# Performance work log

Hardware: AMD Instinct MI355X
Metric: run time of the kernel (lower is better)

The kernel has to match this reference:

```python
import jax, jax.numpy as jnp
import numpy as np

N_NODES = 50000
NUM_FEATURE = 256
NUM_HIDDEN = 128
NUM_CLASSES = 16
N_EDGES = 1600000


def gcn_conv(x, W, b, src, dst, deg_inv_sqrt, n_nodes):
    # GCNConv: h = x @ W ; out[i] = sum_{j->i} norm_ji * h[j] + b
    # with symmetric normalization over the self-loop-augmented graph.
    h = x @ W  # [N, out_ch]
    norm = deg_inv_sqrt[src] * deg_inv_sqrt[dst]  # [E']
    msgs = h[src] * norm[:, None]  # [E', out_ch] (dominant intermediate)
    out = jax.ops.segment_sum(msgs, dst, num_segments=n_nodes)
    return out + b


def setup_inputs() -> dict:
    key = jax.random.key(0)
    k_x, k_e, k_w1, k_b1, k_w2, k_b2 = jax.random.split(key, 6)
    x = jax.random.normal(k_x, (N_NODES, NUM_FEATURE), dtype=jnp.float32)
    edge_index = jax.random.randint(k_e, (2, N_EDGES), 0, N_NODES, dtype=jnp.int64)
    # Glorot init like PyG's GCNConv linear
    s1 = (6.0 / (NUM_FEATURE + NUM_HIDDEN)) ** 0.5
    s2 = (6.0 / (NUM_HIDDEN + NUM_CLASSES)) ** 0.5
    W1 = jax.random.uniform(k_w1, (NUM_FEATURE, NUM_HIDDEN), jnp.float32, -s1, s1)
    b1 = jnp.zeros((NUM_HIDDEN,), jnp.float32)
    W2 = jax.random.uniform(k_w2, (NUM_HIDDEN, NUM_CLASSES), jnp.float32, -s2, s2)
    b2 = jnp.zeros((NUM_CLASSES,), jnp.float32)
    return {"x": x, "edge_index": edge_index, "W1": W1, "b1": b1, "W2": W2, "b2": b2}


def reference(x, edge_index, W1, b1, W2, b2):
    n = x.shape[0]
    # add self-loops (done inside GCNConv for each layer; identical both times)
    loops = jnp.arange(n, dtype=edge_index.dtype)
    src = jnp.concatenate([edge_index[0], loops])
    dst = jnp.concatenate([edge_index[1], loops])
    deg = jax.ops.segment_sum(jnp.ones_like(dst, dtype=x.dtype), dst, num_segments=n)
    deg_inv_sqrt = jnp.where(deg > 0, jax.lax.rsqrt(deg), 0.0)

    h = jax.nn.relu(gcn_conv(x, W1, b1, src, dst, deg_inv_sqrt, n))
    # F.dropout with training=False is the identity (eval-mode baseline)
    logits = gcn_conv(h, W2, b2, src, dst, deg_inv_sqrt, n)
    return jax.nn.log_softmax(logits, axis=1)
```

## Files before the change

kernel.cpp:

```cpp
#include <hip/hip_runtime.h>
#include <hip/hip_fp16.h>
#include <math.h>

#define NF 256
#define NH 128
#define NC 16
#define NB 391
#define NBLK 512

typedef __attribute__((ext_vector_type(8))) short bf16x8;
typedef __attribute__((ext_vector_type(4))) float f32x4;

__device__ __forceinline__ unsigned f2b(float f) {
    unsigned u = __float_as_uint(f);
    return (u + 0x7FFFu + ((u >> 16) & 1u)) >> 16;
}
__device__ __forceinline__ unsigned packt(float a, float b) {
    return (__float_as_uint(a) >> 16) | (__float_as_uint(b) & 0xFFFF0000u);
}
union h2u { __half2 h; unsigned u; };
__device__ __forceinline__ __half2 uh(unsigned u) { h2u c; c.u = u; return c.h; }

__global__ void passA_kernel(const int* __restrict__ dst, int* __restrict__ hist, int E) {
    __shared__ int h[NB];
    for (int i = threadIdx.x; i < NB; i += 256) h[i] = 0;
    __syncthreads();
    int b = blockIdx.x;
    int e0 = (int)((long long)b * E / NBLK), e1 = (int)((long long)(b + 1) * E / NBLK);
    for (int e = e0 + (int)threadIdx.x; e < e1; e += 256)
        atomicAdd(&h[dst[e] >> 7], 1);
    __syncthreads();
    for (int i = threadIdx.x; i < NB; i += 256) hist[b * NB + i] = h[i];
}

__global__ void scanR_kernel(const int* __restrict__ hist, int* __restrict__ bsum) {
    __shared__ int sm[NBLK];
    int k = blockIdx.x, t = threadIdx.x;
    sm[t] = hist[t * NB + k];
    __syncthreads();
    for (int off = NBLK / 2; off > 0; off >>= 1) {
        if (t < off) sm[t] += sm[t + off];
        __syncthreads();
    }
    if (t == 0) bsum[k] = sm[0];
}

__global__ void scanB_kernel(const int* __restrict__ bsum, int* __restrict__ ubase,
                             int* __restrict__ pbase, int N, int E) {
    __shared__ int smu[512];
    __shared__ int smp[512];
    int t = threadIdx.x;
    int vu = (t < NB) ? bsum[t] : 0;
    int vp = (t < NB) ? (((vu + 7) & ~7) + 904) : 0;
    smu[t] = vu; smp[t] = vp;
    __syncthreads();
    for (int off = 1; off < 512; off <<= 1) {
        int uu = (t >= off) ? smu[t - off] : 0;
        int pp = (t >= off) ? smp[t - off] : 0;
        __syncthreads();
        smu[t] += uu; smp[t] += pp;
        __syncthreads();
    }
    if (t < NB) { ubase[t] = smu[t] - vu; pbase[t] = smp[t] - vp; }
    if (t == 0) ubase[NB] = E;
}

__global__ void scanC_kernel(int* __restrict__ hist, const int* __restrict__ ubase) {
    __shared__ int sm[NBLK];
    int k = blockIdx.x, t = threadIdx.x;
    int v = hist[t * NB + k];
    sm[t] = v;
    __syncthreads();
    for (int off = 1; off < NBLK; off <<= 1) {
        int u = (t >= off) ? sm[t - off] : 0;
        __syncthreads();
        sm[t] += u;
        __syncthreads();
    }
    hist[t * NB + k] = ubase[k] + sm[t] - v;
}

__global__ void passB_kernel(const int* __restrict__ src, const int* __restrict__ dst,
                             const int* __restrict__ hist, unsigned* __restrict__ ebuf,
                             int E) {
    __shared__ int cur[NB];
    int b = blockIdx.x;
    for (int i = threadIdx.x; i < NB; i += 256) cur[i] = hist[b * NB + i];
    __syncthreads();
    int e0 = (int)((long long)b * E / NBLK), e1 = (int)((long long)(b + 1) * E / NBLK);
    for (int e = e0 + (int)threadIdx.x; e < e1; e += 256) {
        int d = dst[e];
        int pos = atomicAdd(&cur[d >> 7], 1);
        ebuf[pos] = ((unsigned)d << 16) | (unsigned)src[e];
    }
}

__global__ void passC_kernel(const unsigned* __restrict__ ebuf, const int* __restrict__ ubase,
                             const int* __restrict__ pbase, int* __restrict__ rowptr,
                             int* __restrict__ degs, float* __restrict__ dis,
                             unsigned short* __restrict__ colidx, int N) {
    __shared__ int h[128];
    __shared__ int s2[128];
    __shared__ int curp[128];
    int k = blockIdx.x, t = threadIdx.x;
    if (t < 128) h[t] = 0;
    __syncthreads();
    int e0 = ubase[k], e1 = ubase[k + 1];
    for (int e = e0 + t; e < e1; e += 256)
        atomicAdd(&h[(ebuf[e] >> 16) & 127], 1);
    __syncthreads();
    int v = (t < 128) ? h[t] : 0;
    int pd = (v + 7) & ~7;
    if (t < 128) s2[t] = pd;
    __syncthreads();
    for (int off = 1; off < 128; off <<= 1) {
        int u = (t < 128 && t >= off) ? s2[t - off] : 0;
        __syncthreads();
        if (t < 128) s2[t] += u;
        __syncthreads();
    }
    if (t < 128) {
        int start = pbase[k] + s2[t] - pd;
        int node = k * 128 + t;
        if (node < N) {
            rowptr[node] = start;
            degs[node] = v;
            dis[node] = rsqrtf((float)(v + 1));
        }
        curp[t] = start;
    }
    __syncthreads();
    for (int e = e0 + t; e < e1; e += 256) {
        unsigned w = ebuf[e];
        int dl = (w >> 16) & 127;
        int pos = atomicAdd(&curp[dl], 1);
        colidx[pos] = (unsigned short)(w & 0xFFFFu);
    }
    __syncthreads();
    if (t < 128) {
        int endp = pbase[k] + s2[t];
        for (int q = curp[t]; q < endp; ++q) colidx[q] = (unsigned short)N;
    }
}

__global__ void w1t_kernel(const float* __restrict__ W1, unsigned short* __restrict__ W1T,
                           unsigned* __restrict__ h1T, unsigned* __restrict__ h2sb, int N) {
    int idx = blockIdx.x * 256 + threadIdx.x;
    int n = idx >> 8, k = idx & 255;
    W1T[n * 256 + k] = (unsigned short)f2b(W1[(size_t)k * NH + n]);
    if (idx < 64) {
        int p = idx >> 4, j = idx & 15;
        h1T[(size_t)p * (N + 1) * 16 + (size_t)N * 16 + j] = 0u;
    } else if (idx < 72) {
        h2sb[(size_t)N * 8 + (idx - 64)] = 0u;
    }
}

__global__ __launch_bounds__(256) void gemm1_mfma_kernel(
    const float* __restrict__ x, const unsigned short* __restrict__ W1T,
    const float* __restrict__ dis, unsigned short* __restrict__ h1us, int N) {
    __shared__ char sx[32768];
    int tid = threadIdx.x;
    int wid = tid >> 6, lane = tid & 63;

    for (int it = 0; it < 8; ++it) {
        int lr = it * 4 + wid;
        int grow = blockIdx.x * 32 + lr;
        if (grow >= N) grow = N - 1;
        int fsw = (lr & 7) << 1;
        const char* gp = (const char*)x + (size_t)grow * 1024 + ((lane ^ fsw) << 4);
        __builtin_amdgcn_global_load_lds(gp, sx + lr * 1024 + lane * 16, 16, 0, 0);
    }
    __syncthreads();

    int lrow = lane & 15, lk = lane >> 4;
    int rt = wid & 1, nh = wid >> 1;
    int lr = rt * 16 + lrow;
    int fr = (lr & 7) << 1;
    const float4* lds4 = (const float4*)sx;

    bf16x8 a[8];
#pragma unroll
    for (int kk = 0; kk < 8; ++kk) {
        int v = (kk * 8 + lk * 2) ^ fr;
        float4 lo = lds4[lr * 64 + v];
        float4 hi = lds4[lr * 64 + v + 1];
        union { unsigned u[4]; bf16x8 vv; } av;
        av.u[0] = packt(lo.x, lo.y);
        av.u[1] = packt(lo.z, lo.w);
        av.u[2] = packt(hi.x, hi.y);
        av.u[3] = packt(hi.z, hi.w);
        a[kk] = av.vv;
    }

    f32x4 acc[4];
#pragma unroll
    for (int t = 0; t < 4; ++t) acc[t] = (f32x4){0.f, 0.f, 0.f, 0.f};

#pragma unroll
    for (int nt = 0; nt < 4; ++nt) {
        int n = nh * 64 + nt * 16 + lrow;
        const unsigned short* wp = W1T + (size_t)n * 256 + lk * 8;
        bf16x8 b0 = *(const bf16x8*)(wp + 0 * 32);
        bf16x8 b1 = *(const bf16x8*)(wp + 1 * 32);
        bf16x8 b2 = *(const bf16x8*)(wp + 2 * 32);
        bf16x8 b3 = *(const bf16x8*)(wp + 3 * 32);
        bf16x8 b4 = *(const bf16x8*)(wp + 4 * 32);
        bf16x8 b5 = *(const bf16x8*)(wp + 5 * 32);
        bf16x8 b6 = *(const bf16x8*)(wp + 6 * 32);
        bf16x8 b7 = *(const bf16x8*)(wp + 7 * 32);
        acc[nt] = __builtin_amdgcn_mfma_f32_16x16x32_bf16(a[0], b0, acc[nt], 0, 0, 0);
        acc[nt] = __builtin_amdgcn_mfma_f32_16x16x32_bf16(a[1], b1, acc[nt], 0, 0, 0);
        acc[nt] = __builtin_amdgcn_mfma_f32_16x16x32_bf16(a[2], b2, acc[nt], 0, 0, 0);
        acc[nt] = __builtin_amdgcn_mfma_f32_16x16x32_bf16(a[3], b3, acc[nt], 0, 0, 0);
        acc[nt] = __builtin_amdgcn_mfma_f32_16x16x32_bf16(a[4], b4, acc[nt], 0, 0, 0);
        acc[nt] = __builtin_amdgcn_mfma_f32_16x16x32_bf16(a[5], b5, acc[nt], 0, 0, 0);
        acc[nt] = __builtin_amdgcn_mfma_f32_16x16x32_bf16(a[6], b6, acc[nt], 0, 0, 0);
        acc[nt] = __builtin_amdgcn_mfma_f32_16x16x32_bf16(a[7], b7, acc[nt], 0, 0, 0);
    }

    int rb = blockIdx.x * 32;
    int crow0 = rb + rt * 16 + lk * 4;
#pragma unroll
    for (int r = 0; r < 4; ++r) {
        int row = crow0 + r;
        if (row < N) {
            float dr = dis[row];
#pragma unroll
            for (int nt = 0; nt < 4; ++nt) {
                int p = nh * 2 + (nt >> 1);
                size_t ad = ((size_t)p * (N + 1) + row) * 32 + ((nt & 1) * 16 + lrow);
                __half hv = __float2half(acc[nt][r] * dr);
                h1us[ad] = __half_as_ushort(hv);
            }
        }
    }
}

__global__ __launch_bounds__(256) void aggall_kernel(
    const int* __restrict__ rowptr, const int* __restrict__ degs,
    const unsigned short* __restrict__ colidx,
    const __half2* __restrict__ h1T, __half2* __restrict__ aggT, int N, int bps) {
    int p = blockIdx.x / bps;
    int i = (blockIdx.x - p * bps) * 16 + (threadIdx.x >> 4);
    if (i >= N) return;
    int l = threadIdx.x & 15;
    const __half2* slab = h1T + (size_t)p * (N + 1) * 16;
    __half2 acc = slab[(size_t)i * 16 + l];
    int e = rowptr[i];
    int cnt8 = (degs[i] + 7) >> 3;
    int npair = cnt8 >> 1;
    if (npair > 0) {
        uint4 w0 = *reinterpret_cast<const uint4*>(colidx + e);
        uint4 w1 = *reinterpret_cast<const uint4*>(colidx + e + 8);
        for (int b = 1; b < npair; ++b) {
            uint4 n0 = *reinterpret_cast<const uint4*>(colidx + e + 16 * b);
            uint4 n1 = *reinterpret_cast<const uint4*>(colidx + e + 16 * b + 8);
            int a0 = w0.x & 0xFFFF, a1 = w0.x >> 16, a2 = w0.y & 0xFFFF, a3 = w0.y >> 16;
            int a4 = w0.z & 0xFFFF, a5 = w0.z >> 16, a6 = w0.w & 0xFFFF, a7 = w0.w >> 16;
            int c0 = w1.x & 0xFFFF, c1 = w1.x >> 16, c2 = w1.y & 0xFFFF, c3 = w1.y >> 16;
            int c4 = w1.z & 0xFFFF, c5 = w1.z >> 16, c6 = w1.w & 0xFFFF, c7 = w1.w >> 16;
            __half2 v0 = slab[(size_t)a0 * 16 + l];
            __half2 v1 = slab[(size_t)a1 * 16 + l];
            __half2 v2 = slab[(size_t)a2 * 16 + l];
            __half2 v3 = slab[(size_t)a3 * 16 + l];
            __half2 v4 = slab[(size_t)a4 * 16 + l];
            __half2 v5 = slab[(size_t)a5 * 16 + l];
            __half2 v6 = slab[(size_t)a6 * 16 + l];
            __half2 v7 = slab[(size_t)a7 * 16 + l];
            __half2 u0 = slab[(size_t)c0 * 16 + l];
            __half2 u1 = slab[(size_t)c1 * 16 + l];
            __half2 u2 = slab[(size_t)c2 * 16 + l];
            __half2 u3 = slab[(size_t)c3 * 16 + l];
            __half2 u4 = slab[(size_t)c4 * 16 + l];
            __half2 u5 = slab[(size_t)c5 * 16 + l];
            __half2 u6 = slab[(size_t)c6 * 16 + l];
            __half2 u7 = slab[(size_t)c7 * 16 + l];
            __half2 s0 = __hadd2(__hadd2(v0, v1), __hadd2(v2, v3));
            __half2 s1 = __hadd2(__hadd2(v4, v5), __hadd2(v6, v7));
            __half2 s2 = __hadd2(__hadd2(u0, u1), __hadd2(u2, u3));
            __half2 s3 = __hadd2(__hadd2(u4, u5), __hadd2(u6, u7));
            acc = __hadd2(acc, __hadd2(__hadd2(s0, s1), __hadd2(s2, s3)));
            w0 = n0; w1 = n1;
        }
        {
            int a0 = w0.x & 0xFFFF, a1 = w0.x >> 16, a2 = w0.y & 0xFFFF, a3 = w0.y >> 16;
            int a4 = w0.z & 0xFFFF, a5 = w0.z >> 16, a6 = w0.w & 0xFFFF, a7 = w0.w >> 16;
            int c0 = w1.x & 0xFFFF, c1 = w1.x >> 16, c2 = w1.y & 0xFFFF, c3 = w1.y >> 16;
            int c4 = w1.z & 0xFFFF, c5 = w1.z >> 16, c6 = w1.w & 0xFFFF, c7 = w1.w >> 16;
            __half2 v0 = slab[(size_t)a0 * 16 + l];
            __half2 v1 = slab[(size_t)a1 * 16 + l];
            __half2 v2 = slab[(size_t)a2 * 16 + l];
            __half2 v3 = slab[(size_t)a3 * 16 + l];
            __half2 v4 = slab[(size_t)a4 * 16 + l];
            __half2 v5 = slab[(size_t)a5 * 16 + l];
            __half2 v6 = slab[(size_t)a6 * 16 + l];
            __half2 v7 = slab[(size_t)a7 * 16 + l];
            __half2 u0 = slab[(size_t)c0 * 16 + l];
            __half2 u1 = slab[(size_t)c1 * 16 + l];
            __half2 u2 = slab[(size_t)c2 * 16 + l];
            __half2 u3 = slab[(size_t)c3 * 16 + l];
            __half2 u4 = slab[(size_t)c4 * 16 + l];
            __half2 u5 = slab[(size_t)c5 * 16 + l];
            __half2 u6 = slab[(size_t)c6 * 16 + l];
            __half2 u7 = slab[(size_t)c7 * 16 + l];
            __half2 s0 = __hadd2(__hadd2(v0, v1), __hadd2(v2, v3));
            __half2 s1 = __hadd2(__hadd2(v4, v5), __hadd2(v6, v7));
            __half2 s2 = __hadd2(__hadd2(u0, u1), __hadd2(u2, u3));
            __half2 s3 = __hadd2(__hadd2(u4, u5), __hadd2(u6, u7));
            acc = __hadd2(acc, __hadd2(__hadd2(s0, s1), __hadd2(s2, s3)));
        }
        e += npair * 16;
    }
    if (cnt8 & 1) {
        uint4 w = *reinterpret_cast<const uint4*>(colidx + e);
        int a0 = w.x & 0xFFFF, a1 = w.x >> 16, a2 = w.y & 0xFFFF, a3 = w.y >> 16;
        int a4 = w.z & 0xFFFF, a5 = w.z >> 16, a6 = w.w & 0xFFFF, a7 = w.w >> 16;
        __half2 v0 = slab[(size_t)a0 * 16 + l];
        __half2 v1 = slab[(size_t)a1 * 16 + l];
        __half2 v2 = slab[(size_t)a2 * 16 + l];
        __half2 v3 = slab[(size_t)a3 * 16 + l];
        __half2 v4 = slab[(size_t)a4 * 16 + l];
        __half2 v5 = slab[(size_t)a5 * 16 + l];
        __half2 v6 = slab[(size_t)a6 * 16 + l];
        __half2 v7 = slab[(size_t)a7 * 16 + l];
        __half2 s01 = __hadd2(v0, v1), s23 = __hadd2(v2, v3);
        __half2 s45 = __hadd2(v4, v5), s67 = __hadd2(v6, v7);
        acc = __hadd2(acc, __hadd2(__hadd2(s01, s23), __hadd2(s45, s67)));
    }
    aggT[(size_t)p * N * 16 + (size_t)i * 16 + l] = acc;
}

__global__ __launch_bounds__(256) void relu_gemm2_kernel(
    const __half2* __restrict__ aggT, const float* __restrict__ dis,
    const float* __restrict__ b1, const float* __restrict__ W2,
    __half2* __restrict__ h2sb, int N) {
    __shared__ float sW2[NH * NC];
    __shared__ float srow[4][NH];
    int tid = threadIdx.x;
    for (int k = tid; k < NH * NC; k += 256) sW2[k] = W2[k];
    __syncthreads();

    int wid = tid >> 6, lane = tid & 63;
    int i = blockIdx.x * 4 + wid;
    if (i >= N) return;
    int p = lane >> 4, l16 = lane & 15;
    float2 f = __half22float2(aggT[((size_t)p * N + i) * 16 + l16]);
    float di = dis[i];
    int c0 = p * 32 + l16 * 2;
    srow[wid][c0]     = fmaxf(di * f.x + b1[c0], 0.f);
    srow[wid][c0 + 1] = fmaxf(di * f.y + b1[c0 + 1], 0.f);
    int j = lane & 15, q = lane >> 4;
    const float* rw = srow[wid];
    float pacc = 0.f;
#pragma unroll
    for (int cc = 0; cc < 32; ++cc) {
        int c = q * 32 + cc;
        pacc += rw[c] * sW2[c * NC + j];
    }
    pacc += __shfl_xor(pacc, 16, 64);
    pacc += __shfl_xor(pacc, 32, 64);
    float dp = di * pacc;
    float plo = __shfl(dp, (lane << 1) & 63, 64);
    float phi = __shfl(dp, ((lane << 1) | 1) & 63, 64);
    if (lane < 8) h2sb[(size_t)i * 8 + lane] = __floats2half2_rn(plo, phi);
}

__global__ void layer2_kernel(const int* __restrict__ rowptr, const int* __restrict__ degs,
                              const unsigned short* __restrict__ colidx,
                              const uint2* __restrict__ h2sb2, const float* __restrict__ dis,
                              const float* __restrict__ b2, float* __restrict__ out, int N) {
    int t = blockIdx.x * 256 + threadIdx.x;
    int i = t >> 2;
    if (i >= N) return;
    int j4 = t & 3;
    int e = rowptr[i];
    int cnt4 = (degs[i] + 3) >> 2;
    uint2 sv = h2sb2[(size_t)i * 4 + j4];
    __half2 acc0 = uh(sv.x), acc1 = uh(sv.y);
    if (cnt4 > 0) {
        uint2 w = *reinterpret_cast<const uint2*>(colidx + e);
        for (int b = 1; b < cnt4; ++b) {
            uint2 wn = *reinterpret_cast<const uint2*>(colidx + e + 4 * b);
            int a0 = w.x & 0xFFFF, a1 = w.x >> 16;
            int a2 = w.y & 0xFFFF, a3 = w.y >> 16;
            uint2 g0 = h2sb2[(size_t)a0 * 4 + j4];
            uint2 g1 = h2sb2[(size_t)a1 * 4 + j4];
            uint2 g2 = h2sb2[(size_t)a2 * 4 + j4];
            uint2 g3 = h2sb2[(size_t)a3 * 4 + j4];
            acc0 = __hadd2(acc0, __hadd2(__hadd2(uh(g0.x), uh(g1.x)),
                                         __hadd2(uh(g2.x), uh(g3.x))));
            acc1 = __hadd2(acc1, __hadd2(__hadd2(uh(g0.y), uh(g1.y)),
                                         __hadd2(uh(g2.y), uh(g3.y))));
            w = wn;
        }
        int a0 = w.x & 0xFFFF, a1 = w.x >> 16;
        int a2 = w.y & 0xFFFF, a3 = w.y >> 16;
        uint2 g0 = h2sb2[(size_t)a0 * 4 + j4];
        uint2 g1 = h2sb2[(size_t)a1 * 4 + j4];
        uint2 g2 = h2sb2[(size_t)a2 * 4 + j4];
        uint2 g3 = h2sb2[(size_t)a3 * 4 + j4];
        acc0 = __hadd2(acc0, __hadd2(__hadd2(uh(g0.x), uh(g1.x)),
                                     __hadd2(uh(g2.x), uh(g3.x))));
        acc1 = __hadd2(acc1, __hadd2(__hadd2(uh(g0.y), uh(g1.y)),
                                     __hadd2(uh(g2.y), uh(g3.y))));
    }
    float2 f0 = __half22float2(acc0);
    float2 f1 = __half22float2(acc1);
    float di = dis[i];
    float4 bb = *reinterpret_cast<const float4*>(b2 + 4 * j4);
    float l0 = di * f0.x + bb.x;
    float l1 = di * f0.y + bb.y;
    float l2 = di * f1.x + bb.z;
    float l3 = di * f1.y + bb.w;
    float m = fmaxf(fmaxf(l0, l1), fmaxf(l2, l3));
    m = fmaxf(m, __shfl_xor(m, 1, 64));
    m = fmaxf(m, __shfl_xor(m, 2, 64));
    float s = __expf(l0 - m) + __expf(l1 - m) + __expf(l2 - m) + __expf(l3 - m);
    s += __shfl_xor(s, 1, 64);
    s += __shfl_xor(s, 2, 64);
    float lse = m + __logf(s);
    float4 o = make_float4(l0 - lse, l1 - lse, l2 - lse, l3 - lse);
    *reinterpret_cast<float4*>(out + (size_t)i * NC + 4 * j4) = o;
}

extern "C" void kernel_launch(void* const* d_in, const int* in_sizes, int n_in,
                              void* d_out, int out_size, void* d_ws, size_t ws_size,
                              hipStream_t stream) {
    const float* x  = (const float*)d_in[0];
    const int*   ei = (const int*)d_in[1];
    const float* W1 = (const float*)d_in[2];
    const float* b1 = (const float*)d_in[3];
    const float* W2 = (const float*)d_in[4];
    const float* b2 = (const float*)d_in[5];
    float* out = (float*)d_out;

    const int N = in_sizes[0] / NF;
    const int E = in_sizes[1] / 2;
    const int* src = ei;
    const int* dst = ei + E;

    __half2*        h1T    = (__half2*)d_ws;
    __half2*        aggT   = h1T + (size_t)4 * (N + 1) * 16;
    __half2*        h2sb   = aggT + (size_t)4 * N * 16;
    float*          dis    = (float*)(h2sb + (size_t)(N + 1) * 8);
    int*            degs   = (int*)(dis + N);
    int*            rowptr = degs + N;
    int*            hist   = rowptr + N;
    int*            bsum   = hist + NBLK * NB;
    int*            ubase  = bsum + NB;
    int*            pbase  = ubase + NB + 1;
    unsigned*       ebuf   = (unsigned*)(pbase + NB + 1);
    unsigned short* colidx = (unsigned short*)(ebuf + E);
    unsigned short* W1T    = (unsigned short*)ebuf;

    passA_kernel<<<NBLK, 256, 0, stream>>>(dst, hist, E);
    scanR_kernel<<<NB, NBLK, 0, stream>>>(hist, bsum);
    scanB_kernel<<<1, 512, 0, stream>>>(bsum, ubase, pbase, N, E);
    scanC_kernel<<<NB, NBLK, 0, stream>>>(hist, ubase);
    passB_kernel<<<NBLK, 256, 0, stream>>>(src, dst, hist, ebuf, E);
    passC_kernel<<<NB, 256, 0, stream>>>(ebuf, ubase, pbase, rowptr, degs, dis, colidx, N);

    w1t_kernel<<<128, 256, 0, stream>>>(W1, W1T, (unsigned*)h1T, (unsigned*)h2sb, N);

    gemm1_mfma_kernel<<<(N + 31) / 32, 256, 0, stream>>>(x, W1T, dis,
                                                         (unsigned short*)h1T, N);

    const int bps = (N + 15) / 16;
    aggall_kernel<<<4 * bps, 256, 0, stream>>>(rowptr, degs, colidx, h1T, aggT, N, bps);

    relu_gemm2_kernel<<<(N + 3) / 4, 256, 0, stream>>>(aggT, dis, b1, W2, h2sb, N);

    layer2_kernel<<<((size_t)N * 4 + 255) / 256, 256, 0, stream>>>(rowptr, degs, colidx,
                                                                   (const uint2*)h2sb, dis, b2, out, N);
}
```

Before: 164.4 us.

## Pre-convert x to fp16 in fused prep kernel and use f16 MFMA GEMM1

Merges the edge histogram pass and the W1 transpose into one prep launch, which also converts x to fp16 into workspace when space allows. GEMM1 then reads half-width x and uses f16 MFMA instead of converting fp32 x itself. The x conversion overlaps with the histogram blocks and is meant to halve GEMM1's input traffic and cut one launch. The cost is an extra full read and write of x, an fp16 range/precision risk, and a fallback that depends on the workspace size.

Result: no change. 166.5 us (+1.3%).

```diff
diff --git a/kernel.cpp b/kernel.cpp
--- a/kernel.cpp
+++ b/kernel.cpp
@@ -7,8 +7,10 @@
 #define NC 16
 #define NB 391
 #define NBLK 512
+#define XCB 512
 
 typedef __attribute__((ext_vector_type(8))) short bf16x8;
+typedef __attribute__((ext_vector_type(8))) _Float16 f16x8;
 typedef __attribute__((ext_vector_type(4))) float f32x4;
 
 __device__ __forceinline__ unsigned f2b(float f) {
@@ -20,17 +22,44 @@
 }
 union h2u { __half2 h; unsigned u; };
 __device__ __forceinline__ __half2 uh(unsigned u) { h2u c; c.u = u; return c.h; }
-
-__global__ void passA_kernel(const int* __restrict__ dst, int* __restrict__ hist, int E) {
+__device__ __forceinline__ unsigned hu(__half2 h) { h2u c; c.h = h; return c.u; }
+
+__global__ void prep_kernel(const int* __restrict__ dst, int* __restrict__ hist, int E,
+                            const float* __restrict__ W1, unsigned short* __restrict__ W1T,
+                            unsigned* __restrict__ h1T, unsigned* __restrict__ h2sb,
+                            const float* __restrict__ x, uint2* __restrict__ xh,
+                            int N, int C4, int fast) {
     __shared__ int h[NB];
-    for (int i = threadIdx.x; i < NB; i += 256) h[i] = 0;
-    __syncthreads();
-    int b = blockIdx.x;
-    int e0 = (int)((long long)b * E / NBLK), e1 = (int)((long long)(b + 1) * E / NBLK);
-    for (int e = e0 + (int)threadIdx.x; e < e1; e += 256)
-        atomicAdd(&h[dst[e] >> 7], 1);
-    __syncthreads();
-    for (int i = threadIdx.x; i < NB; i += 256) hist[b * NB + i] = h[i];
+    int b = blockIdx.x, tid = threadIdx.x;
+    if (b < NBLK) {
+        for (int i = tid; i < NB; i += 256) h[i] = 0;
+        __syncthreads();
+        int e0 = (int)((long long)b * E / NBLK), e1 = (int)((long long)(b + 1) * E / NBLK);
+        for (int e = e0 + tid; e < e1; e += 256)
+            atomicAdd(&h[dst[e] >> 7], 1);
+        __syncthreads();
+        for (int i = tid; i < NB; i += 256) hist[b * NB + i] = h[i];
+    } else if (b < NBLK + 128) {
+        int idx = (b - NBLK) * 256 + tid;
+        int n = idx >> 8, k = idx & 255;
+        float w = W1[(size_t)k * NH + n];
+        W1T[n * 256 + k] = fast ? __half_as_ushort(__float2half(w))
+                                : (unsigned short)f2b(w);
+        if (idx < 64) {
+            int p = idx >> 4, j = idx & 15;
+            h1T[(size_t)p * (N + 1) * 16 + (size_t)N * 16 + j] = 0u;
+        } else if (idx < 72) {
+            h2sb[(size_t)N * 8 + (idx - 64)] = 0u;
+        }
+    } else if (fast) {
+        int i = (b - NBLK - 128) * 256 + tid;
+        const float4* x4 = (const float4*)x;
+        for (; i < C4; i += XCB * 256) {
+            float4 v = x4[i];
+            xh[i] = make_uint2(hu(__floats2half2_rn(v.x, v.y)),
+                               hu(__floats2half2_rn(v.z, v.w)));
+        }
+    }
 }
 
 __global__ void scanR_kernel(const int* __restrict__ hist, int* __restrict__ bsum) {
@@ -143,20 +172,81 @@
     }
 }
 
-__global__ void w1t_kernel(const float* __restrict__ W1, unsigned short* __restrict__ W1T,
-                           unsigned* __restrict__ h1T, unsigned* __restrict__ h2sb, int N) {
-    int idx = blockIdx.x * 256 + threadIdx.x;
-    int n = idx >> 8, k = idx & 255;
-    W1T[n * 256 + k] = (unsigned short)f2b(W1[(size_t)k * NH + n]);
-    if (idx < 64) {
-        int p = idx >> 4, j = idx & 15;
-        h1T[(size_t)p * (N + 1) * 16 + (size_t)N * 16 + j] = 0u;
-    } else if (idx < 72) {
-        h2sb[(size_t)N * 8 + (idx - 64)] = 0u;
-    }
-}
-
-__global__ __launch_bounds__(256) void gemm1_mfma_kernel(
+__global__ __launch_bounds__(256) void gemm1_f16_kernel(
+    const unsigned short* __restrict__ xh, const unsigned short* __restrict__ W1T,
+    const float* __restrict__ dis, unsigned short* __restrict__ h1us, int N) {
+    __shared__ char sx[16384];
+    int tid = threadIdx.x;
+    int wid = tid >> 6, lane = tid & 63;
+
+    for (int it = 0; it < 4; ++it) {
+        int rp = (it * 4 + wid) * 2;
+        int row = rp + (lane >> 5);
+        int grow = blockIdx.x * 32 + row;
+        if (grow >= N) grow = N - 1;
+        int u = (lane & 31) ^ (row & 7);
+        const char* gp = (const char*)(xh + (size_t)grow * 256) + (u << 4);
+        __builtin_amdgcn_global_load_lds(gp, sx + rp * 512 + lane * 16, 16, 0, 0);
+    }
+    __syncthreads();
+
+    int lrow = lane & 15, lk = lane >> 4;
+    int rt = wid & 1, nh = wid >> 1;
+    int lr = rt * 16 + lrow;
+    int sw = lr & 7;
+
+    f16x8 a[8];
+#pragma unroll
+    for (int kk = 0; kk < 8; ++kk) {
+        int u = (kk * 4 + lk) ^ sw;
+        a[kk] = *(const f16x8*)(sx + lr * 512 + u * 16);
+    }
+
+    f32x4 acc[4];
+#pragma unroll
+    for (int t = 0; t < 4; ++t) acc[t] = (f32x4){0.f, 0.f, 0.f, 0.f};
+
+#pragma unroll
+    for (int nt = 0; nt < 4; ++nt) {
+        int n = nh * 64 + nt * 16 + lrow;
+        const unsigned short* wp = W1T + (size_t)n * 256 + lk * 8;
+        f16x8 b0 = *(const f16x8*)(wp + 0 * 32);
+        f16x8 b1 = *(const f16x8*)(wp + 1 * 32);
+        f16x8 b2 = *(const f16x8*)(wp + 2 * 32);
+        f16x8 b3 = *(const f16x8*)(wp + 3 * 32);
+        f16x8 b4 = *(const f16x8*)(wp + 4 * 32);
+        f16x8 b5 = *(const f16x8*)(wp + 5 * 32);
+        f16x8 b6 = *(const f16x8*)(wp + 6 * 32);
+        f16x8 b7 = *(const f16x8*)(wp + 7 * 32);
+        acc[nt] = __builtin_amdgcn_mfma_f32_16x16x32_f16(a[0], b0, acc[nt], 0, 0, 0);
+        acc[nt] = __builtin_amdgcn_mfma_f32_16x16x32_f16(a[1], b1, acc[nt], 0, 0, 0);
+        acc[nt] = __builtin_amdgcn_mfma_f32_16x16x32_f16(a[2], b2, acc[nt], 0, 0, 0);
+        acc[nt] = __builtin_amdgcn_mfma_f32_16x16x32_f16(a[3], b3, acc[nt], 0, 0, 0);
+        acc[nt] = __builtin_amdgcn_mfma_f32_16x16x32_f16(a[4], b4, acc[nt], 0, 0, 0);
+        acc[nt] = __builtin_amdgcn_mfma_f32_16x16x32_f16(a[5], b5, acc[nt], 0, 0, 0);
+        acc[nt] = __builtin_amdgcn_mfma_f32_16x16x32_f16(a[6], b6, acc[nt], 0, 0, 0);
+        acc[nt] = __builtin_amdgcn_mfma_f32_16x16x32_f16(a[7], b7, acc[nt], 0, 0, 0);
+    }
+
+    int rb = blockIdx.x * 32;
+    int crow0 = rb + rt * 16 + lk * 4;
+#pragma unroll
+    for (int r = 0; r < 4; ++r) {
+        int row = crow0 + r;
+        if (row < N) {
+            float dr = dis[row];
+#pragma unroll
+            for (int nt = 0; nt < 4; ++nt) {
+                int p = nh * 2 + (nt >> 1);
+                size_t ad = ((size_t)p * (N + 1) + row) * 32 + ((nt & 1) * 16 + lrow);
+                __half hv = __float2half(acc[nt][r] * dr);
+                h1us[ad] = __half_as_ushort(hv);
+            }
+        }
+    }
+}
+
+__global__ __launch_bounds__(256) void gemm1_f32_kernel(
     const float* __restrict__ x, const unsigned short* __restrict__ W1T,
     const float* __restrict__ dis, unsigned short* __restrict__ h1us, int N) {
     __shared__ char sx[32768];
@@ -452,19 +542,28 @@
     int*            pbase  = ubase + NB + 1;
     unsigned*       ebuf   = (unsigned*)(pbase + NB + 1);
     unsigned short* colidx = (unsigned short*)(ebuf + E);
-    unsigned short* W1T    = (unsigned short*)ebuf;
-
-    passA_kernel<<<NBLK, 256, 0, stream>>>(dst, hist, E);
+    unsigned short* W1T    = colidx + (size_t)E + 360000;
+    size_t off_xh = (((size_t)((char*)(W1T + 32768) - (char*)d_ws)) + 15) & ~(size_t)15;
+    unsigned short* xh     = (unsigned short*)((char*)d_ws + off_xh);
+    size_t need_fast = off_xh + (size_t)N * 256 * sizeof(unsigned short);
+    int fast = (ws_size >= need_fast) ? 1 : 0;
+    const int C4 = N * NF / 4;
+
+    prep_kernel<<<NBLK + 128 + XCB, 256, 0, stream>>>(dst, hist, E, W1, W1T,
+                                                      (unsigned*)h1T, (unsigned*)h2sb,
+                                                      x, (uint2*)xh, N, C4, fast);
     scanR_kernel<<<NB, NBLK, 0, stream>>>(hist, bsum);
     scanB_kernel<<<1, 512, 0, stream>>>(bsum, ubase, pbase, N, E);
     scanC_kernel<<<NB, NBLK, 0, stream>>>(hist, ubase);
     passB_kernel<<<NBLK, 256, 0, stream>>>(src, dst, hist, ebuf, E);
     passC_kernel<<<NB, 256, 0, stream>>>(ebuf, ubase, pbase, rowptr, degs, dis, colidx, N);
 
-    w1t_kernel<<<128, 256, 0, stream>>>(W1, W1T, (unsigned*)h1T, (unsigned*)h2sb, N);
-
-    gemm1_mfma_kernel<<<(N + 31) / 32, 256, 0, stream>>>(x, W1T, dis,
-                                                         (unsigned short*)h1T, N);
+    if (fast)
+        gemm1_f16_kernel<<<(N + 31) / 32, 256, 0, stream>>>(xh, W1T, dis,
+                                                            (unsigned short*)h1T, N);
+    else
+        gemm1_f32_kernel<<<(N + 31) / 32, 256, 0, stream>>>(x, W1T, dis,
+                                                            (unsigned short*)h1T, N);
 
     const int bps = (N + 15) / 16;
     aggall_kernel<<<4 * bps, 256, 0, stream>>>(rowptr, degs, colidx, h1T, aggT, N, bps);
```
